# Kernel optimization log

Hardware: AMD Instinct MI355X
Metric: run time of the kernel (lower is better)

## Reference

```python
import jax, jax.numpy as jnp
import numpy as np

N_BINS = 64
SIGMA_SCALE = 0.5
EPS = 1e-8


def _radial_weights(H, W, dtype=jnp.float32):
    r_max = min(H, W) / 2.0 - 1.0
    yy, xx = jnp.meshgrid(jnp.arange(H, dtype=dtype), jnp.arange(W, dtype=dtype), indexing='ij')
    cx, cy = (W - 1) / 2.0, (H - 1) / 2.0
    r = jnp.sqrt((xx - cx) ** 2 + (yy - cy) ** 2)  # (H, W)
    edges = jnp.linspace(0.0, r_max, N_BINS + 1, dtype=dtype)
    centers = 0.5 * (edges[:-1] + edges[1:])  # (B,)
    bin_width = r_max / N_BINS
    sigma = SIGMA_SCALE * bin_width + EPS
    Wmat = jnp.exp(-0.5 * ((r[:, :, None] - centers) / sigma) ** 2)  # (H, W, B)
    return Wmat, centers


def setup_inputs() -> dict:
    key = jax.random.key(0)
    k1, k2 = jax.random.split(key)
    shape = (32, 12, 256, 256)
    pred = jax.random.uniform(k1, shape, dtype=jnp.float32)
    target = jax.random.uniform(k2, shape, dtype=jnp.float32)
    return {"pred": pred, "target": target}


def reference(pred, target):
    N, WVL, H, W = pred.shape
    Wmat, centers = _radial_weights(H, W, pred.dtype)
    Wflat = Wmat.reshape(H * W, N_BINS)            # (HW, B)
    den = jnp.maximum(Wflat.sum(axis=0), EPS)      # (B,)
    # broadcast-multiply-reduce expressed as a GEMM: (N*WVL, HW) @ (HW, B)
    Xf = pred.reshape(N, WVL, H * W)
    Yf = target.reshape(N, WVL, H * W)
    prof_pred = jnp.einsum('nwp,pb->nwb', Xf, Wflat) / den
    prof_targ = jnp.einsum('nwp,pb->nwb', Yf, Wflat) / den
    # bin_weight == 'r': weight by bin-center radius, normalized to unit mean
    w = centers[None, None, :]
    w = w / jnp.maximum(w.mean(axis=-1, keepdims=True), EPS)  # (1,1,B)
    # loss == 'fvu'
    y = prof_targ
    ybar = y.mean(axis=-1, keepdims=True)
    sse = (w * (prof_pred - y) ** 2).sum(axis=-1)
    ssy = jnp.maximum((w * (y - ybar) ** 2).sum(axis=-1), EPS)
    return (sse / ssy).mean()
```

## Files before the change

### kernel.cpp

```cpp
#include <hip/hip_runtime.h>
#include <math.h>


#define NBINS 64
#define WIN   8
#define G     2
#define NIMG  384
#define HDIM  256
#define WDIM  256
#define BANDS 16
#define BANDROWS 16

#define DEN_BANDS 128
#define DEN_ROWS  2

#define LOG2E 1.4426950408889634f
#define EXP_M4 0.018315638888734179f

__device__ __forceinline__ float fexp2(float x) {
#if __has_builtin(__builtin_amdgcn_exp2f)
  return __builtin_amdgcn_exp2f(x);
#else
  return exp2f(x);
#endif
}

__global__ __launch_bounds__(256) void radial_prof_kernel(
    const float* __restrict__ pred,
    const float* __restrict__ targ,
    float* __restrict__ prof)
{
  const int x     = threadIdx.x;
  const int band  = blockIdx.x & (BANDS - 1);
  const int chunk = blockIdx.x >> 4;
  const int g0    = chunk * G;

  __shared__ float hist[G][2][NBINS];
  for (int i = threadIdx.x; i < G * 2 * NBINS; i += 256) ((float*)hist)[i] = 0.f;
  __syncthreads();

  const float dx     = (float)x - 127.5f;
  const float dx2    = dx * dx;
  const int   y0     = band * BANDROWS;
  const float inv_bw = 64.0f / 127.0f;

  float acc[G][2][WIN];
  #pragma unroll
  for (int g = 0; g < G; ++g)
    #pragma unroll
    for (int i = 0; i < 2; ++i)
      #pragma unroll
      for (int s = 0; s < WIN; ++s) acc[g][i][s] = 0.f;

  float dy  = (float)y0 - 127.5f;
  float rsq = dx2 + dy * dy;
  int k0 = (int)floorf(sqrtf(rsq) * inv_bw) - 3;

  const size_t istr = (size_t)HDIM * WDIM;
  const float* pp = pred + (size_t)g0 * istr + (size_t)y0 * WDIM + x;
  const float* tp = targ + (size_t)g0 * istr + (size_t)y0 * WDIM + x;

  for (int yi = 0; yi < BANDROWS; ++yi) {
    const float u  = sqrtf(rsq) * inv_bw;
    const float fl = floorf(u);
    const int   k  = (int)fl - 3;
    rsq += 2.0f * dy + 1.0f;
    dy  += 1.0f;

    if (k != k0) {
      if (k == k0 + 1) {
        if ((unsigned)k0 < NBINS) {
          #pragma unroll
          for (int g = 0; g < G; ++g) {
            atomicAdd(&hist[g][0][k0], acc[g][0][0]);
            atomicAdd(&hist[g][1][k0], acc[g][1][0]);
          }
        }
        #pragma unroll
        for (int g = 0; g < G; ++g)
          #pragma unroll
          for (int i = 0; i < 2; ++i) {
            #pragma unroll
            for (int s = 0; s < WIN - 1; ++s) acc[g][i][s] = acc[g][i][s + 1];
            acc[g][i][WIN - 1] = 0.f;
          }
      } else if (k == k0 - 1) {
        const int bh = k0 + WIN - 1;
        if ((unsigned)bh < NBINS) {
          #pragma unroll
          for (int g = 0; g < G; ++g) {
            atomicAdd(&hist[g][0][bh], acc[g][0][WIN - 1]);
            atomicAdd(&hist[g][1][bh], acc[g][1][WIN - 1]);
          }
        }
        #pragma unroll
        for (int g = 0; g < G; ++g)
          #pragma unroll
          for (int i = 0; i < 2; ++i) {
            #pragma unroll
            for (int s = WIN - 1; s > 0; --s) acc[g][i][s] = acc[g][i][s - 1];
            acc[g][i][0] = 0.f;
          }
      } else {
        #pragma unroll
        for (int s = 0; s < WIN; ++s) {
          const int b = k0 + s;
          if ((unsigned)b < NBINS) {
            #pragma unroll
            for (int g = 0; g < G; ++g) {
              atomicAdd(&hist[g][0][b], acc[g][0][s]);
              atomicAdd(&hist[g][1][b], acc[g][1][s]);
            }
          }
        }
        #pragma unroll
        for (int g = 0; g < G; ++g)
          #pragma unroll
          for (int i = 0; i < 2; ++i)
            #pragma unroll
            for (int s = 0; s < WIN; ++s) acc[g][i][s] = 0.f;
      }
      k0 = k;
    }

    if (k0 < NBINS) {
      const float t0 = (u - fl) + 2.5f;
      float w = fexp2(-(2.0f * LOG2E) * t0 * t0);
      float m = fexp2((4.0f * t0 - 2.0f) * LOG2E);
      float xp[G], xt[G];
      #pragma unroll
      for (int g = 0; g < G; ++g) {
        xp[g] = pp[(size_t)g * istr];
        xt[g] = tp[(size_t)g * istr];
      }
      #pragma unroll
      for (int s = 0; s < WIN; ++s) {
        #pragma unroll
        for (int g = 0; g < G; ++g) {
          acc[g][0][s] = fmaf(w, xp[g], acc[g][0][s]);
          acc[g][1][s] = fmaf(w, xt[g], acc[g][1][s]);
        }
        w *= m;
        m *= EXP_M4;
      }
    }
    pp += WDIM; tp += WDIM;
  }

  #pragma unroll
  for (int s = 0; s < WIN; ++s) {
    const int b = k0 + s;
    if ((unsigned)b < NBINS) {
      #pragma unroll
      for (int g = 0; g < G; ++g) {
        atomicAdd(&hist[g][0][b], acc[g][0][s]);
        atomicAdd(&hist[g][1][b], acc[g][1][s]);
      }
    }
  }
  __syncthreads();

  for (int i = threadIdx.x; i < G * 2 * NBINS; i += 256)
    atomicAdd(&prof[(size_t)g0 * 2 * NBINS + i], ((float*)hist)[i]);
}

__global__ __launch_bounds__(256) void den_kernel(float* __restrict__ den)
{
  const int x    = threadIdx.x;
  const int band = blockIdx.x;
  __shared__ float hist[NBINS];
  if (threadIdx.x < NBINS) hist[threadIdx.x] = 0.f;
  __syncthreads();

  const float dx     = (float)x - 127.5f;
  const float dx2    = dx * dx;
  const int   y0     = band * DEN_ROWS;
  const float inv_bw = 64.0f / 127.0f;

  float acc[WIN];
  #pragma unroll
  for (int s = 0; s < WIN; ++s) acc[s] = 0.f;

  int k0;
  {
    const float dy = (float)y0 - 127.5f;
    k0 = (int)floorf(sqrtf(dx2 + dy * dy) * inv_bw) - 3;
  }

  for (int yi = 0; yi < DEN_ROWS; ++yi) {
    const float dy = (float)(y0 + yi) - 127.5f;
    const float r  = sqrtf(dx2 + dy * dy);
    const float u  = r * inv_bw;
    const float fl = floorf(u);
    const int   k  = (int)fl - 3;

    if (k != k0) {
      if (k == k0 + 1) {
        if ((unsigned)k0 < NBINS) atomicAdd(&hist[k0], acc[0]);
        #pragma unroll
        for (int s = 0; s < WIN - 1; ++s) acc[s] = acc[s + 1];
        acc[WIN - 1] = 0.f;
      } else if (k == k0 - 1) {
        const int bh = k0 + WIN - 1;
        if ((unsigned)bh < NBINS) atomicAdd(&hist[bh], acc[WIN - 1]);
        #pragma unroll
        for (int s = WIN - 1; s > 0; --s) acc[s] = acc[s - 1];
        acc[0] = 0.f;
      } else {
        #pragma unroll
        for (int s = 0; s < WIN; ++s) {
          const int b = k0 + s;
          if ((unsigned)b < NBINS) atomicAdd(&hist[b], acc[s]);
          acc[s] = 0.f;
        }
      }
      k0 = k;
    }

    if (k0 < NBINS) {
      const float t0 = (u - fl) + 2.5f;
      float w = fexp2(-(2.0f * LOG2E) * t0 * t0);
      float m = fexp2((4.0f * t0 - 2.0f) * LOG2E);
      #pragma unroll
      for (int s = 0; s < WIN; ++s) {
        acc[s] += w;
        w *= m;
        m *= EXP_M4;
      }
    }
  }

  #pragma unroll
  for (int s = 0; s < WIN; ++s) {
    const int b = k0 + s;
    if ((unsigned)b < NBINS) atomicAdd(&hist[b], acc[s]);
  }
  __syncthreads();
  if (threadIdx.x < NBINS) atomicAdd(&den[threadIdx.x], hist[threadIdx.x]);
}

__global__ __launch_bounds__(NIMG) void loss_kernel(
    const float* __restrict__ prof,
    const float* __restrict__ den,
    float* __restrict__ out)
{
  __shared__ float dsh[NBINS];
  __shared__ float red[NIMG];
  const int tid = threadIdx.x;
  if (tid < NBINS) dsh[tid] = 1.0f / fmaxf(den[tid], 1e-8f);
  __syncthreads();

  const float bw = 127.0f / 64.0f;
  const float* base = prof + (size_t)tid * (2 * NBINS);

  float tsum = 0.f;
  for (int b = 0; b < NBINS; ++b) tsum += base[NBINS + b] * dsh[b];
  const float ybar = tsum * (1.0f / NBINS);

  float sse = 0.f, ssy = 0.f;
  for (int b = 0; b < NBINS; ++b) {
    const float wb = ((float)b + 0.5f) * bw * (1.0f / 63.5f);
    const float P  = base[b] * dsh[b];
    const float T  = base[NBINS + b] * dsh[b];
    const float d1 = P - T;
    const float d2 = T - ybar;
    sse = fmaf(wb * d1, d1, sse);
    ssy = fmaf(wb * d2, d2, ssy);
  }
  red[tid] = sse / fmaxf(ssy, 1e-8f);
  __syncthreads();

  for (int s = 256; s > 0; s >>= 1) {
    if (tid < s && tid + s < NIMG) red[tid] += red[tid + s];
    __syncthreads();
  }
  if (tid == 0) out[0] = red[0] * (1.0f / NIMG);
}

extern "C" void kernel_launch(void* const* d_in, const int* in_sizes, int n_in,
                              void* d_out, int out_size, void* d_ws, size_t ws_size,
                              hipStream_t stream) {
  const float* pred = (const float*)d_in[0];
  const float* targ = (const float*)d_in[1];

  float* prof = (float*)d_ws;
  float* den  = prof + (size_t)NIMG * 2 * NBINS;

  hipMemsetAsync(d_ws, 0, ((size_t)NIMG * 2 * NBINS + NBINS) * sizeof(float), stream);

  den_kernel<<<DEN_BANDS, 256, 0, stream>>>(den);
  radial_prof_kernel<<<(NIMG / G) * BANDS, 256, 0, stream>>>(pred, targ, prof);
  loss_kernel<<<1, NIMG, 0, stream>>>(prof, den, (float*)d_out);
}
```

Measured before the change: 380.3 us.

## Replace sliding bin window with fixed 4-row chunks and 9-wide padded histogram

The per-row sliding-window accumulator with its divergent shift and flush branches is replaced by fixed 4-row chunks. Each chunk anchors a 9-bin window at the minimum floor radius and flushes it unconditionally into an LDS histogram padded with guard slots, which removes the bounds checks. The denominator kernel follows the same scheme, and the loss kernel becomes a wavefront-per-image shuffle reduction with atomic accumulation into the output. This trades branch divergence and serial row dependence for more atomics per chunk and a slightly wider window. The 9-wide window assumes the radius varies by at most about one bin within 4 rows.

```diff
diff --git a/kernel.cpp b/kernel.cpp
--- a/kernel.cpp
+++ b/kernel.cpp
@@ -3,16 +3,17 @@
 
 
 #define NBINS 64
-#define WIN   8
+#define S     9
 #define G     2
 #define NIMG  384
 #define HDIM  256
 #define WDIM  256
 #define BANDS 16
 #define BANDROWS 16
-
-#define DEN_BANDS 128
-#define DEN_ROWS  2
+#define CHUNK 4
+#define NCHUNK (BANDROWS / CHUNK)
+#define GUARD 4
+#define HSLOTS 80
 
 #define LOG2E 1.4426950408889634f
 #define EXP_M4 0.018315638888734179f
@@ -30,251 +31,170 @@
     const float* __restrict__ targ,
     float* __restrict__ prof)
 {
-  const int x     = threadIdx.x;
-  const int band  = blockIdx.x & (BANDS - 1);
-  const int chunk = blockIdx.x >> 4;
-  const int g0    = chunk * G;
-
-  __shared__ float hist[G][2][NBINS];
-  for (int i = threadIdx.x; i < G * 2 * NBINS; i += 256) ((float*)hist)[i] = 0.f;
+  const int x    = threadIdx.x;
+  const int band = blockIdx.x & (BANDS - 1);
+  const int gi   = blockIdx.x >> 4;
+  const int g0   = gi * G;
+
+  __shared__ float hist[G][2][HSLOTS];
+  for (int i = threadIdx.x; i < G * 2 * HSLOTS; i += 256) ((float*)hist)[i] = 0.f;
   __syncthreads();
 
   const float dx     = (float)x - 127.5f;
-  const float dx2    = dx * dx;
   const int   y0     = band * BANDROWS;
   const float inv_bw = 64.0f / 127.0f;
 
-  float acc[G][2][WIN];
-  #pragma unroll
-  for (int g = 0; g < G; ++g)
-    #pragma unroll
-    for (int i = 0; i < 2; ++i)
-      #pragma unroll
-      for (int s = 0; s < WIN; ++s) acc[g][i][s] = 0.f;
-
   float dy  = (float)y0 - 127.5f;
-  float rsq = dx2 + dy * dy;
-  int k0 = (int)floorf(sqrtf(rsq) * inv_bw) - 3;
+  float rsq = dx * dx + dy * dy;
 
   const size_t istr = (size_t)HDIM * WDIM;
-  const float* pp = pred + (size_t)g0 * istr + (size_t)y0 * WDIM + x;
-  const float* tp = targ + (size_t)g0 * istr + (size_t)y0 * WDIM + x;
-
-  for (int yi = 0; yi < BANDROWS; ++yi) {
-    const float u  = sqrtf(rsq) * inv_bw;
-    const float fl = floorf(u);
-    const int   k  = (int)fl - 3;
+  const float* pbase = pred + (size_t)g0 * istr + (size_t)y0 * WDIM + x;
+  const float* tbase = targ + (size_t)g0 * istr + (size_t)y0 * WDIM + x;
+
+  for (int c = 0; c < NCHUNK; ++c) {
+    float u[CHUNK];
+    #pragma unroll
+    for (int r = 0; r < CHUNK; ++r) {
+      u[r] = sqrtf(rsq) * inv_bw;
+      rsq += 2.0f * dy + 1.0f;
+      dy  += 1.0f;
+    }
+    const float fm = fminf(floorf(u[0]), floorf(u[CHUNK - 1]));
+    const int   kb = (int)fm - 3;
+
+    if (kb < NBINS) {
+      float dp0[CHUNK], dp1[CHUNK], dt0[CHUNK], dt1[CHUNK];
+      #pragma unroll
+      for (int r = 0; r < CHUNK; ++r) {
+        dp0[r] = pbase[r * WDIM];
+        dp1[r] = pbase[r * WDIM + istr];
+        dt0[r] = tbase[r * WDIM];
+        dt1[r] = tbase[r * WDIM + istr];
+      }
+
+      float acc[G][2][S];
+      #pragma unroll
+      for (int g = 0; g < G; ++g)
+        #pragma unroll
+        for (int t = 0; t < 2; ++t)
+          #pragma unroll
+          for (int j = 0; j < S; ++j) acc[g][t][j] = 0.f;
+
+      #pragma unroll
+      for (int r = 0; r < CHUNK; ++r) {
+        const float T = (u[r] - fm) + 2.5f;
+        float w = fexp2(-(2.0f * LOG2E) * T * T);
+        float m = fexp2((4.0f * T - 2.0f) * LOG2E);
+        #pragma unroll
+        for (int j = 0; j < S; ++j) {
+          acc[0][0][j] = fmaf(w, dp0[r], acc[0][0][j]);
+          acc[0][1][j] = fmaf(w, dt0[r], acc[0][1][j]);
+          acc[1][0][j] = fmaf(w, dp1[r], acc[1][0][j]);
+          acc[1][1][j] = fmaf(w, dt1[r], acc[1][1][j]);
+          w *= m;
+          m *= EXP_M4;
+        }
+      }
+
+      #pragma unroll
+      for (int j = 0; j < S; ++j) {
+        const int bp = kb + GUARD + j;
+        atomicAdd(&hist[0][0][bp], acc[0][0][j]);
+        atomicAdd(&hist[0][1][bp], acc[0][1][j]);
+        atomicAdd(&hist[1][0][bp], acc[1][0][j]);
+        atomicAdd(&hist[1][1][bp], acc[1][1][j]);
+      }
+    }
+    pbase += CHUNK * WDIM;
+    tbase += CHUNK * WDIM;
+  }
+  __syncthreads();
+
+  {
+    const int i = threadIdx.x;
+    const int g = i >> 7, t = (i >> 6) & 1, b = i & 63;
+    atomicAdd(&prof[((size_t)(g0 + g) * 2 + t) * NBINS + b], hist[g][t][b + GUARD]);
+  }
+}
+
+__global__ __launch_bounds__(256) void den_kernel(float* __restrict__ den)
+{
+  const int x  = threadIdx.x;
+  const int y0 = blockIdx.x * CHUNK;
+
+  __shared__ float hist[HSLOTS];
+  if (threadIdx.x < HSLOTS) hist[threadIdx.x] = 0.f;
+  __syncthreads();
+
+  const float dx     = (float)x - 127.5f;
+  const float inv_bw = 64.0f / 127.0f;
+  float dy  = (float)y0 - 127.5f;
+  float rsq = dx * dx + dy * dy;
+
+  float u[CHUNK];
+  #pragma unroll
+  for (int r = 0; r < CHUNK; ++r) {
+    u[r] = sqrtf(rsq) * inv_bw;
     rsq += 2.0f * dy + 1.0f;
     dy  += 1.0f;
-
-    if (k != k0) {
-      if (k == k0 + 1) {
-        if ((unsigned)k0 < NBINS) {
-          #pragma unroll
-          for (int g = 0; g < G; ++g) {
-            atomicAdd(&hist[g][0][k0], acc[g][0][0]);
-            atomicAdd(&hist[g][1][k0], acc[g][1][0]);
-          }
-        }
-        #pragma unroll
-        for (int g = 0; g < G; ++g)
-          #pragma unroll
-          for (int i = 0; i < 2; ++i) {
-            #pragma unroll
-            for (int s = 0; s < WIN - 1; ++s) acc[g][i][s] = acc[g][i][s + 1];
-            acc[g][i][WIN - 1] = 0.f;
-          }
-      } else if (k == k0 - 1) {
-        const int bh = k0 + WIN - 1;
-        if ((unsigned)bh < NBINS) {
-          #pragma unroll
-          for (int g = 0; g < G; ++g) {
-            atomicAdd(&hist[g][0][bh], acc[g][0][WIN - 1]);
-            atomicAdd(&hist[g][1][bh], acc[g][1][WIN - 1]);
-          }
-        }
-        #pragma unroll
-        for (int g = 0; g < G; ++g)
-          #pragma unroll
-          for (int i = 0; i < 2; ++i) {
-            #pragma unroll
-            for (int s = WIN - 1; s > 0; --s) acc[g][i][s] = acc[g][i][s - 1];
-            acc[g][i][0] = 0.f;
-          }
-      } else {
-        #pragma unroll
-        for (int s = 0; s < WIN; ++s) {
-          const int b = k0 + s;
-          if ((unsigned)b < NBINS) {
-            #pragma unroll
-            for (int g = 0; g < G; ++g) {
-              atomicAdd(&hist[g][0][b], acc[g][0][s]);
-              atomicAdd(&hist[g][1][b], acc[g][1][s]);
-            }
-          }
-        }
-        #pragma unroll
-        for (int g = 0; g < G; ++g)
-          #pragma unroll
-          for (int i = 0; i < 2; ++i)
-            #pragma unroll
-            for (int s = 0; s < WIN; ++s) acc[g][i][s] = 0.f;
-      }
-      k0 = k;
-    }
-
-    if (k0 < NBINS) {
-      const float t0 = (u - fl) + 2.5f;
-      float w = fexp2(-(2.0f * LOG2E) * t0 * t0);
-      float m = fexp2((4.0f * t0 - 2.0f) * LOG2E);
-      float xp[G], xt[G];
-      #pragma unroll
-      for (int g = 0; g < G; ++g) {
-        xp[g] = pp[(size_t)g * istr];
-        xt[g] = tp[(size_t)g * istr];
-      }
-      #pragma unroll
-      for (int s = 0; s < WIN; ++s) {
-        #pragma unroll
-        for (int g = 0; g < G; ++g) {
-          acc[g][0][s] = fmaf(w, xp[g], acc[g][0][s]);
-          acc[g][1][s] = fmaf(w, xt[g], acc[g][1][s]);
-        }
+  }
+  const float fm = fminf(floorf(u[0]), floorf(u[CHUNK - 1]));
+  const int   kb = (int)fm - 3;
+
+  if (kb < NBINS) {
+    float acc[S];
+    #pragma unroll
+    for (int j = 0; j < S; ++j) acc[j] = 0.f;
+    #pragma unroll
+    for (int r = 0; r < CHUNK; ++r) {
+      const float T = (u[r] - fm) + 2.5f;
+      float w = fexp2(-(2.0f * LOG2E) * T * T);
+      float m = fexp2((4.0f * T - 2.0f) * LOG2E);
+      #pragma unroll
+      for (int j = 0; j < S; ++j) {
+        acc[j] += w;
         w *= m;
         m *= EXP_M4;
       }
     }
-    pp += WDIM; tp += WDIM;
-  }
-
-  #pragma unroll
-  for (int s = 0; s < WIN; ++s) {
-    const int b = k0 + s;
-    if ((unsigned)b < NBINS) {
-      #pragma unroll
-      for (int g = 0; g < G; ++g) {
-        atomicAdd(&hist[g][0][b], acc[g][0][s]);
-        atomicAdd(&hist[g][1][b], acc[g][1][s]);
-      }
-    }
-  }
-  __syncthreads();
-
-  for (int i = threadIdx.x; i < G * 2 * NBINS; i += 256)
-    atomicAdd(&prof[(size_t)g0 * 2 * NBINS + i], ((float*)hist)[i]);
-}
-
-__global__ __launch_bounds__(256) void den_kernel(float* __restrict__ den)
-{
-  const int x    = threadIdx.x;
-  const int band = blockIdx.x;
-  __shared__ float hist[NBINS];
-  if (threadIdx.x < NBINS) hist[threadIdx.x] = 0.f;
-  __syncthreads();
-
-  const float dx     = (float)x - 127.5f;
-  const float dx2    = dx * dx;
-  const int   y0     = band * DEN_ROWS;
-  const float inv_bw = 64.0f / 127.0f;
-
-  float acc[WIN];
-  #pragma unroll
-  for (int s = 0; s < WIN; ++s) acc[s] = 0.f;
-
-  int k0;
-  {
-    const float dy = (float)y0 - 127.5f;
-    k0 = (int)floorf(sqrtf(dx2 + dy * dy) * inv_bw) - 3;
-  }
-
-  for (int yi = 0; yi < DEN_ROWS; ++yi) {
-    const float dy = (float)(y0 + yi) - 127.5f;
-    const float r  = sqrtf(dx2 + dy * dy);
-    const float u  = r * inv_bw;
-    const float fl = floorf(u);
-    const int   k  = (int)fl - 3;
-
-    if (k != k0) {
-      if (k == k0 + 1) {
-        if ((unsigned)k0 < NBINS) atomicAdd(&hist[k0], acc[0]);
-        #pragma unroll
-        for (int s = 0; s < WIN - 1; ++s) acc[s] = acc[s + 1];
-        acc[WIN - 1] = 0.f;
-      } else if (k == k0 - 1) {
-        const int bh = k0 + WIN - 1;
-        if ((unsigned)bh < NBINS) atomicAdd(&hist[bh], acc[WIN - 1]);
-        #pragma unroll
-        for (int s = WIN - 1; s > 0; --s) acc[s] = acc[s - 1];
-        acc[0] = 0.f;
-      } else {
-        #pragma unroll
-        for (int s = 0; s < WIN; ++s) {
-          const int b = k0 + s;
-          if ((unsigned)b < NBINS) atomicAdd(&hist[b], acc[s]);
-          acc[s] = 0.f;
-        }
-      }
-      k0 = k;
-    }
-
-    if (k0 < NBINS) {
-      const float t0 = (u - fl) + 2.5f;
-      float w = fexp2(-(2.0f * LOG2E) * t0 * t0);
-      float m = fexp2((4.0f * t0 - 2.0f) * LOG2E);
-      #pragma unroll
-      for (int s = 0; s < WIN; ++s) {
-        acc[s] += w;
-        w *= m;
-        m *= EXP_M4;
-      }
-    }
-  }
-
-  #pragma unroll
-  for (int s = 0; s < WIN; ++s) {
-    const int b = k0 + s;
-    if ((unsigned)b < NBINS) atomicAdd(&hist[b], acc[s]);
-  }
-  __syncthreads();
-  if (threadIdx.x < NBINS) atomicAdd(&den[threadIdx.x], hist[threadIdx.x]);
-}
-
-__global__ __launch_bounds__(NIMG) void loss_kernel(
+    #pragma unroll
+    for (int j = 0; j < S; ++j) atomicAdd(&hist[kb + GUARD + j], acc[j]);
+  }
+  __syncthreads();
+  if (threadIdx.x < NBINS) atomicAdd(&den[threadIdx.x], hist[threadIdx.x + GUARD]);
+}
+
+__global__ __launch_bounds__(256) void loss_kernel(
     const float* __restrict__ prof,
     const float* __restrict__ den,
     float* __restrict__ out)
 {
-  __shared__ float dsh[NBINS];
-  __shared__ float red[NIMG];
-  const int tid = threadIdx.x;
-  if (tid < NBINS) dsh[tid] = 1.0f / fmaxf(den[tid], 1e-8f);
-  __syncthreads();
-
-  const float bw = 127.0f / 64.0f;
-  const float* base = prof + (size_t)tid * (2 * NBINS);
-
-  float tsum = 0.f;
-  for (int b = 0; b < NBINS; ++b) tsum += base[NBINS + b] * dsh[b];
-  const float ybar = tsum * (1.0f / NBINS);
-
-  float sse = 0.f, ssy = 0.f;
-  for (int b = 0; b < NBINS; ++b) {
-    const float wb = ((float)b + 0.5f) * bw * (1.0f / 63.5f);
-    const float P  = base[b] * dsh[b];
-    const float T  = base[NBINS + b] * dsh[b];
-    const float d1 = P - T;
-    const float d2 = T - ybar;
-    sse = fmaf(wb * d1, d1, sse);
-    ssy = fmaf(wb * d2, d2, ssy);
-  }
-  red[tid] = sse / fmaxf(ssy, 1e-8f);
-  __syncthreads();
-
-  for (int s = 256; s > 0; s >>= 1) {
-    if (tid < s && tid + s < NIMG) red[tid] += red[tid + s];
-    __syncthreads();
-  }
-  if (tid == 0) out[0] = red[0] * (1.0f / NIMG);
+  const int wid  = threadIdx.x >> 6;
+  const int lane = threadIdx.x & 63;
+  const int img  = blockIdx.x * 4 + wid;
+
+  const float inv_d = 1.0f / fmaxf(den[lane], 1e-8f);
+  const float* base = prof + (size_t)img * 2 * NBINS;
+  const float P = base[lane] * inv_d;
+  const float T = base[NBINS + lane] * inv_d;
+
+  float s = T;
+  #pragma unroll
+  for (int off = 32; off > 0; off >>= 1) s += __shfl_xor(s, off);
+  const float ybar = s * (1.0f / NBINS);
+
+  const float wb = ((float)lane + 0.5f) * (1.0f / 32.0f);
+  const float d1 = P - T;
+  const float d2 = T - ybar;
+  float sse = wb * d1 * d1;
+  float ssy = wb * d2 * d2;
+  #pragma unroll
+  for (int off = 32; off > 0; off >>= 1) sse += __shfl_xor(sse, off);
+  #pragma unroll
+  for (int off = 32; off > 0; off >>= 1) ssy += __shfl_xor(ssy, off);
+
+  if (lane == 0)
+    atomicAdd(out, (sse / fmaxf(ssy, 1e-8f)) * (1.0f / NIMG));
 }
 
 extern "C" void kernel_launch(void* const* d_in, const int* in_sizes, int n_in,
@@ -287,8 +207,9 @@
   float* den  = prof + (size_t)NIMG * 2 * NBINS;
 
   hipMemsetAsync(d_ws, 0, ((size_t)NIMG * 2 * NBINS + NBINS) * sizeof(float), stream);
-
-  den_kernel<<<DEN_BANDS, 256, 0, stream>>>(den);
+  hipMemsetAsync(d_out, 0, sizeof(float), stream);
+
+  den_kernel<<<HDIM / CHUNK, 256, 0, stream>>>(den);
   radial_prof_kernel<<<(NIMG / G) * BANDS, 256, 0, stream>>>(pred, targ, prof);
-  loss_kernel<<<1, NIMG, 0, stream>>>(prof, den, (float*)d_out);
-}
+  loss_kernel<<<NIMG / 4, 256, 0, stream>>>(prof, den, (float*)d_out);
+}
```

Measured after the change: 828.9 us. 2.18x slower.
